# Optimization experiments

Measured on AMD Instinct MI355X. Metric: run time of the kernel, lower is better.

## Reference

```python
import math
import jax, jax.numpy as jnp
import numpy as np

B, H, D, N, M = 4, 8, 64, 8192, 256
EPS = 1e-6


def sample_orthogonal_random_vectors(num_rows, num_cols, seed=0):
    """Faithful port of FavorAttention.sample_orthogonal_random_vectors."""
    rng = np.random.default_rng(seed)
    num_blocks = math.ceil(num_rows / num_cols)
    unstructured = rng.standard_normal((num_blocks, num_cols, num_cols)).astype(np.float32)
    norm = np.linalg.norm(unstructured, axis=-1).reshape(-1, 1)
    q, _ = np.linalg.qr(unstructured)                 # reduced QR per block
    q = np.transpose(q, (0, 2, 1)).reshape(-1, num_cols)
    q = q[:num_rows, :] * norm[:num_rows, :]
    return jnp.asarray(q, dtype=jnp.float32)


def setup_inputs() -> dict:
    key = jax.random.key(0)
    kq, kk, kv = jax.random.split(key, 3)
    return {
        "query": jax.random.normal(kq, (B, H, D, N), dtype=jnp.float32),
        "key": jax.random.normal(kk, (B, H, D, N), dtype=jnp.float32),
        "value": jax.random.normal(kv, (B, H, D, N), dtype=jnp.float32),
        "projection_matrix": sample_orthogonal_random_vectors(M, D),
    }


def randomized_kernel(x, proj, is_query, eps=EPS):
    """FAVOR+ positive softmax features. x: [B,H,D,N] -> phi: [B,H,M,N]."""
    d = x.shape[2]
    data_normalizer = d ** -0.25
    ratio = proj.shape[0] ** -0.5
    # projected: [B,H,M,N]
    u = jnp.einsum('md,bhdn->bhmn', proj, x) * data_normalizer
    # ||x||^2 / (2*sqrt(d)) per token: [B,H,1,N]
    diag = jnp.sum(x * x, axis=2, keepdims=True) * (data_normalizer ** 2) * 0.5
    if is_query:
        stab = jnp.max(u, axis=2, keepdims=True)            # per-token max over features
    else:
        stab = jnp.max(u, axis=(2, 3), keepdims=True)       # global max per (b,h)
    return ratio * (jnp.exp(u - diag - stab) + eps)


def reference(query, key, value, projection_matrix):
    q_phi = randomized_kernel(query, projection_matrix, is_query=True)    # [B,H,M,N]
    k_phi = randomized_kernel(key, projection_matrix, is_query=False)     # [B,H,M,N]
    # kv = key @ value^T over sequence: [B,H,M,D]
    kv = jnp.einsum('bhmn,bhdn->bhmd', k_phi, value)
    key_norm = jnp.sum(k_phi, axis=3)                                     # [B,H,M]
    out = jnp.einsum('bhmn,bhmd->bhnd', q_phi, kv)                        # [B,H,N,D]
    out_norm = jnp.einsum('bhmn,bhm->bhn', q_phi, key_norm)[..., None]    # [B,H,N,1]
    out = out / out_norm
    return jnp.swapaxes(out, 2, 3)                                        # [B,H,D,N]


if __name__ == '__main__':
    o = reference(**setup_inputs())
    print(o.shape, o.dtype)
```

## Files before the change

### kernel.cpp

```cpp
#include <hip/hip_runtime.h>


typedef short s16x8 __attribute__((ext_vector_type(8)));
typedef float f32x4 __attribute__((ext_vector_type(4)));

#define Dv 64
#define Nv 8192
#define Mv 256
#define BHv 32
#define SPL 16
#define NSPL (Nv / SPL)
#define NCH (NSPL / 64)

#define DNRM 0.3535533905932738f
#define EPSV 1e-6f
#define KSTAB 15.0f

#define OFF_SGM 0
#define OFF_SVP (OFF_SGM + BHv * SPL * 8)
#define OFF_KNP (OFF_SVP + BHv * SPL * 64)
#define OFF_KNF (OFF_KNP + BHv * SPL * Mv)
#define OFF_KVP (OFF_KNF + BHv * Mv)
#define OFF_KVT (OFF_KVP + BHv * SPL * Mv * Dv)

__device__ __forceinline__ unsigned short f2b(float x) {
    return __builtin_bit_cast(unsigned short, (__bf16)x);
}

__device__ __forceinline__ s16x8 load_pfrag(const float* __restrict__ proj, int m,
                                            int kc, int q) {
    const float* p = proj + m * 64 + kc * 32 + q * 8;
    s16x8 r;
#pragma unroll
    for (int j = 0; j < 8; ++j) r[j] = (short)f2b(p[j]);
    return r;
}

__global__ __launch_bounds__(512, 4) void favor_kv(const float* __restrict__ key,
                                                   const float* __restrict__ value,
                                                   const float* __restrict__ proj,
                                                   float* __restrict__ ws) {
    __shared__ __align__(16) unsigned short KT[64][72];
    __shared__ __align__(16) unsigned short VL[64][72];
    __shared__ __align__(16) unsigned short PH[256][40];
    __shared__ __align__(16) float dred[16][64];
    __shared__ __align__(16) float dgl[64];
    const int tid = threadIdx.x;
    const int w = tid >> 6, l = tid & 63, c = l & 15, q = l >> 4;
    const int sg = tid >> 4, cs = tid & 15;
    const int s = blockIdx.x, bh = blockIdx.y;
    const float* kp = key + (size_t)bh * Dv * Nv;
    const float* vp = value + (size_t)bh * Dv * Nv;

    s16x8 P[2][2];
#pragma unroll
    for (int mt = 0; mt < 2; ++mt)
#pragma unroll
        for (int kc = 0; kc < 2; ++kc)
            P[mt][kc] = load_pfrag(proj, (2 * w + mt) * 16 + c, kc, q);

    f32x4 kva[2][4];
#pragma unroll
    for (int mt = 0; mt < 2; ++mt)
#pragma unroll
        for (int dt = 0; dt < 4; ++dt) kva[mt][dt] = (f32x4){0.f, 0.f, 0.f, 0.f};
    float kn[2] = {0.f, 0.f};
    float sv[4] = {0.f, 0.f, 0.f, 0.f};
    float tmax = -3.0e38f;

    for (int ch = 0; ch < NCH; ++ch) {
        const int n0 = s * NSPL + ch * 64;
        if (ch) __syncthreads();
        if (sg < 16) {
            const int g = sg;
            float4 kk[4];
#pragma unroll
            for (int di = 0; di < 4; ++di)
                kk[di] = *(const float4*)&kp[(4 * g + di) * Nv + n0 + 4 * cs];
#pragma unroll
            for (int j = 0; j < 4; ++j) {
                const float k0 = ((const float*)&kk[0])[j];
                const float k1 = ((const float*)&kk[1])[j];
                const float k2 = ((const float*)&kk[2])[j];
                const float k3 = ((const float*)&kk[3])[j];
                *(short4*)&KT[4 * cs + j][4 * g] =
                    make_short4((short)f2b(k0), (short)f2b(k1), (short)f2b(k2),
                                (short)f2b(k3));
                dred[g][4 * cs + j] = (k0 * k0 + k1 * k1) + (k2 * k2 + k3 * k3);
            }
        } else {
            const int g2 = sg - 16;
            float4 vv[4];
#pragma unroll
            for (int di = 0; di < 4; ++di)
                vv[di] = *(const float4*)&vp[(4 * g2 + di) * Nv + n0 + 4 * cs];
#pragma unroll
            for (int di = 0; di < 4; ++di) {
                *(short4*)&VL[4 * g2 + di][4 * cs] = make_short4(
                    (short)f2b(vv[di].x), (short)f2b(vv[di].y),
                    (short)f2b(vv[di].z), (short)f2b(vv[di].w));
                sv[di] += (vv[di].x + vv[di].y) + (vv[di].z + vv[di].w);
            }
        }
        __syncthreads();
        if (tid < 64) {
            float ds = 0.f;
#pragma unroll
            for (int gg = 0; gg < 16; ++gg) ds += dred[gg][tid];
            dgl[tid] = ds * 0.0625f + KSTAB;
        }
        __syncthreads();
#pragma unroll
        for (int h = 0; h < 2; ++h) {
#pragma unroll
            for (int nt2 = 0; nt2 < 2; ++nt2) {
                const int nt = 2 * h + nt2;
                const s16x8 a0 = *(const s16x8*)&KT[nt * 16 + c][q * 8];
                const s16x8 a1 = *(const s16x8*)&KT[nt * 16 + c][32 + q * 8];
                const float4 dg = *(const float4*)&dgl[nt * 16 + q * 4];
#pragma unroll
                for (int mt = 0; mt < 2; ++mt) {
                    f32x4 u = {0.f, 0.f, 0.f, 0.f};
                    u = __builtin_amdgcn_mfma_f32_16x16x32_bf16(a0, P[mt][0], u, 0, 0, 0);
                    u = __builtin_amdgcn_mfma_f32_16x16x32_bf16(a1, P[mt][1], u, 0, 0, 0);
                    tmax = fmaxf(tmax, fmaxf(fmaxf(u[0], u[1]), fmaxf(u[2], u[3])));
                    const float e0 = __expf(__builtin_fmaf(u[0], DNRM, -dg.x));
                    const float e1 = __expf(__builtin_fmaf(u[1], DNRM, -dg.y));
                    const float e2 = __expf(__builtin_fmaf(u[2], DNRM, -dg.z));
                    const float e3 = __expf(__builtin_fmaf(u[3], DNRM, -dg.w));
                    kn[mt] += (e0 + e1) + (e2 + e3);
                    *(short4*)&PH[(2 * w + mt) * 16 + c][nt2 * 16 + q * 4] =
                        make_short4((short)f2b(e0), (short)f2b(e1),
                                    (short)f2b(e2), (short)f2b(e3));
                }
            }
            s16x8 bf[4];
#pragma unroll
            for (int dt = 0; dt < 4; ++dt)
                bf[dt] = *(const s16x8*)&VL[dt * 16 + c][h * 32 + q * 8];
#pragma unroll
            for (int mt = 0; mt < 2; ++mt) {
                const s16x8 a = *(const s16x8*)&PH[(2 * w + mt) * 16 + c][q * 8];
#pragma unroll
                for (int dt = 0; dt < 4; ++dt)
                    kva[mt][dt] = __builtin_amdgcn_mfma_f32_16x16x32_bf16(
                        a, bf[dt], kva[mt][dt], 0, 0, 0);
            }
        }
    }
#pragma unroll
    for (int off = 1; off < 64; off <<= 1)
        tmax = fmaxf(tmax, __shfl_xor(tmax, off, 64));
    if (l == 0) ws[OFF_SGM + (bh * SPL + s) * 8 + w] = tmax * DNRM;
    float* kvp = ws + OFF_KVP + (size_t)(bh * SPL + s) * Mv * Dv;
#pragma unroll
    for (int mt = 0; mt < 2; ++mt) {
        const int mrow = (2 * w + mt) * 16 + 4 * q;
#pragma unroll
        for (int dt = 0; dt < 4; ++dt) {
            const int dcol = dt * 16 + c;
#pragma unroll
            for (int r = 0; r < 4; ++r)
                kvp[(size_t)(mrow + r) * Dv + dcol] = kva[mt][dt][r];
        }
    }
#pragma unroll
    for (int mt = 0; mt < 2; ++mt) {
        kn[mt] += __shfl_xor(kn[mt], 16, 64);
        kn[mt] += __shfl_xor(kn[mt], 32, 64);
    }
    if (q == 0) {
        float* knp = ws + OFF_KNP + (bh * SPL + s) * Mv;
#pragma unroll
        for (int mt = 0; mt < 2; ++mt) knp[(2 * w + mt) * 16 + c] = kn[mt];
    }
    __syncthreads();
    float* sp = &dred[0][0];
    if (sg >= 16) {
        const int g2 = sg - 16;
#pragma unroll
        for (int di = 0; di < 4; ++di) sp[(4 * g2 + di) * 16 + cs] = sv[di];
    }
    __syncthreads();
    if (tid < 64) {
        float t2 = 0.f;
#pragma unroll
        for (int j = 0; j < 16; ++j) t2 += sp[tid * 16 + j];
        ws[OFF_SVP + (bh * SPL + s) * 64 + tid] = t2;
    }
}

__global__ __launch_bounds__(256) void favor_kvred(float* __restrict__ ws) {
    __shared__ float sAl;
    __shared__ float svl[64];
    const int t = threadIdx.x, f = blockIdx.x, bh = blockIdx.y;
    const int flat = f * 1024 + t * 4;
    const int m = flat >> 6, d0 = flat & 63;
    if (t < 64) {
        float v = fmaxf(ws[OFF_SGM + bh * 128 + t],
                        ws[OFF_SGM + bh * 128 + 64 + t]);
#pragma unroll
        for (int off = 1; off < 64; off <<= 1)
            v = fmaxf(v, __shfl_xor(v, off, 64));
        if (t == 0) sAl = __expf(KSTAB - v);
    } else if (t < 128) {
        const int d = t - 64;
        float x = 0.f;
#pragma unroll
        for (int s2 = 0; s2 < SPL; ++s2)
            x += ws[OFF_SVP + (bh * SPL + s2) * 64 + d];
        svl[d] = x;
    }
    __syncthreads();
    const float al = sAl;
    float4 acc = make_float4(0.f, 0.f, 0.f, 0.f);
    for (int s2 = 0; s2 < SPL; ++s2) {
        const float4 v =
            *(const float4*)&ws[OFF_KVP + ((size_t)(bh * SPL + s2) << 14) + flat];
        acc.x += v.x; acc.y += v.y; acc.z += v.z; acc.w += v.w;
    }
    acc.x = acc.x * al + EPSV * svl[d0 + 0];
    acc.y = acc.y * al + EPSV * svl[d0 + 1];
    acc.z = acc.z * al + EPSV * svl[d0 + 2];
    acc.w = acc.w * al + EPSV * svl[d0 + 3];
    unsigned short* kvT = (unsigned short*)(ws + OFF_KVT);
    kvT[(bh * 64 + d0 + 0) * 256 + m] = f2b(acc.x);
    kvT[(bh * 64 + d0 + 1) * 256 + m] = f2b(acc.y);
    kvT[(bh * 64 + d0 + 2) * 256 + m] = f2b(acc.z);
    kvT[(bh * 64 + d0 + 3) * 256 + m] = f2b(acc.w);
    if (t < 16) {
        const int mm = f * 16 + t;
        float kk = 0.f;
        for (int s2 = 0; s2 < SPL; ++s2)
            kk += ws[OFF_KNP + (bh * SPL + s2) * Mv + mm];
        ws[OFF_KNF + bh * Mv + mm] = kk * al + EPSV * (float)Nv;
    }
}

__global__ __launch_bounds__(256, 2) void favor_out(const float* __restrict__ query,
                                                    const float* __restrict__ proj,
                                                    const float* __restrict__ ws,
                                                    float* __restrict__ out) {
    __shared__ __align__(16) unsigned short PHT[64][264];
    __shared__ float npart[4][64];
    __shared__ float knl[256];
    __shared__ float cw[4][64];
    __shared__ float stabl[64];
    __shared__ float dql[64];
    unsigned short (*QT)[72] = (unsigned short (*)[72]) & PHT[0][0];
    float (*dred)[64] = (float (*)[64])((char*)&PHT[0][0] + 9216);
    const int tid = threadIdx.x;
    const int w = tid >> 6, l = tid & 63, c = l & 15, q = l >> 4;
    const int g = tid >> 4, cs = tid & 15;
    const int nb = blockIdx.x, bh = blockIdx.y;
    const int n0 = nb * 64;
    const float* qp = query + (size_t)bh * Dv * Nv;
    const unsigned short* kvT =
        (const unsigned short*)(ws + OFF_KVT) + (size_t)bh * 64 * 256;

    {
        float4 qq[4];
#pragma unroll
        for (int di = 0; di < 4; ++di)
            qq[di] = *(const float4*)&qp[(4 * g + di) * Nv + n0 + 4 * cs];
#pragma unroll
        for (int j = 0; j < 4; ++j) {
            const float v0 = ((const float*)&qq[0])[j];
            const float v1 = ((const float*)&qq[1])[j];
            const float v2 = ((const float*)&qq[2])[j];
            const float v3 = ((const float*)&qq[3])[j];
            *(short4*)&QT[4 * cs + j][4 * g] =
                make_short4((short)f2b(v0), (short)f2b(v1), (short)f2b(v2),
                            (short)f2b(v3));
            dred[g][4 * cs + j] = (v0 * v0 + v1 * v1) + (v2 * v2 + v3 * v3);
        }
    }
    knl[tid] = ws[OFF_KNF + bh * Mv + tid];

    s16x8 P[4][2];
#pragma unroll
    for (int mt = 0; mt < 4; ++mt)
#pragma unroll
        for (int kc = 0; kc < 2; ++kc)
            P[mt][kc] = load_pfrag(proj, (4 * w + mt) * 16 + c, kc, q);
    __syncthreads();

    f32x4 u[4][4];
#pragma unroll
    for (int mt = 0; mt < 4; ++mt)
#pragma unroll
        for (int nt = 0; nt < 4; ++nt) u[mt][nt] = (f32x4){0.f, 0.f, 0.f, 0.f};
#pragma unroll
    for (int nt = 0; nt < 4; ++nt) {
        const s16x8 b0 = *(const s16x8*)&QT[nt * 16 + c][q * 8];
        const s16x8 b1 = *(const s16x8*)&QT[nt * 16 + c][32 + q * 8];
#pragma unroll
        for (int mt = 0; mt < 4; ++mt) {
            u[mt][nt] =
                __builtin_amdgcn_mfma_f32_16x16x32_bf16(P[mt][0], b0, u[mt][nt], 0, 0, 0);
            u[mt][nt] =
                __builtin_amdgcn_mfma_f32_16x16x32_bf16(P[mt][1], b1, u[mt][nt], 0, 0, 0);
        }
    }
#pragma unroll
    for (int nt = 0; nt < 4; ++nt) {
        float vm = -3.4e38f;
#pragma unroll
        for (int mt = 0; mt < 4; ++mt)
            vm = fmaxf(vm, fmaxf(fmaxf(u[mt][nt][0], u[mt][nt][1]),
                                 fmaxf(u[mt][nt][2], u[mt][nt][3])));
        vm = fmaxf(vm, __shfl_xor(vm, 16, 64));
        vm = fmaxf(vm, __shfl_xor(vm, 32, 64));
        if (q == 0) cw[w][nt * 16 + c] = vm;
    }
    __syncthreads();
    if (tid < 64) {
        stabl[tid] =
            fmaxf(fmaxf(cw[0][tid], cw[1][tid]), fmaxf(cw[2][tid], cw[3][tid]));
        float dsum = 0.f;
#pragma unroll
        for (int gg = 0; gg < 16; ++gg) dsum += dred[gg][tid];
        dql[tid] = dsum * 0.0625f;
    }
    __syncthreads();
#pragma unroll
    for (int nt = 0; nt < 4; ++nt) {
        const float sr = stabl[nt * 16 + c];
        const float dq = dql[nt * 16 + c];
        float np = 0.f;
#pragma unroll
        for (int mt = 0; mt < 4; ++mt) {
            const float e0 = __expf((u[mt][nt][0] - sr) * DNRM - dq) + EPSV;
            const float e1 = __expf((u[mt][nt][1] - sr) * DNRM - dq) + EPSV;
            const float e2 = __expf((u[mt][nt][2] - sr) * DNRM - dq) + EPSV;
            const float e3 = __expf((u[mt][nt][3] - sr) * DNRM - dq) + EPSV;
            const int mb = (4 * w + mt) * 16 + 4 * q;
            np += e0 * knl[mb] + e1 * knl[mb + 1] + e2 * knl[mb + 2] +
                  e3 * knl[mb + 3];
            *(short4*)&PHT[nt * 16 + c][mb] = make_short4(
                (short)f2b(e0), (short)f2b(e1), (short)f2b(e2), (short)f2b(e3));
        }
        np += __shfl_xor(np, 16, 64);
        np += __shfl_xor(np, 32, 64);
        if (q == 0) npart[w][nt * 16 + c] = np;
    }
    __syncthreads();
    f32x4 acc[4];
#pragma unroll
    for (int dt = 0; dt < 4; ++dt) acc[dt] = (f32x4){0.f, 0.f, 0.f, 0.f};
#pragma unroll
    for (int kc = 0; kc < 8; ++kc) {
        const s16x8 a = *(const s16x8*)&PHT[w * 16 + c][kc * 32 + q * 8];
#pragma unroll
        for (int dt = 0; dt < 4; ++dt) {
            const s16x8 b =
                *(const s16x8*)&kvT[(size_t)(dt * 16 + c) * 256 + kc * 32 + q * 8];
            acc[dt] = __builtin_amdgcn_mfma_f32_16x16x32_bf16(a, b, acc[dt], 0, 0, 0);
        }
    }
    __syncthreads();
    float* ot = (float*)&PHT[0][0];
    float rn[4];
#pragma unroll
    for (int r = 0; r < 4; ++r) {
        const int nl = w * 16 + 4 * q + r;
        rn[r] = 1.0f / ((npart[0][nl] + npart[1][nl]) +
                        (npart[2][nl] + npart[3][nl]));
    }
#pragma unroll
    for (int dt = 0; dt < 4; ++dt)
#pragma unroll
        for (int r = 0; r < 4; ++r)
            ot[(dt * 16 + c) * 68 + (w * 16 + 4 * q + r)] = acc[dt][r] * rn[r];
    __syncthreads();
    float* op = out + (size_t)bh * Dv * Nv;
    {
        const int d = tid >> 2, ng = (tid & 3) * 16;
#pragma unroll
        for (int i = 0; i < 4; ++i) {
            const float4 v = *(const float4*)&ot[d * 68 + ng + i * 4];
            *(float4*)&op[d * Nv + n0 + ng + i * 4] = v;
        }
    }
}

extern "C" void kernel_launch(void* const* d_in, const int* in_sizes, int n_in,
                              void* d_out, int out_size, void* d_ws, size_t ws_size,
                              hipStream_t stream) {
    const float* q = (const float*)d_in[0];
    const float* k = (const float*)d_in[1];
    const float* v = (const float*)d_in[2];
    const float* proj = (const float*)d_in[3];
    float* ws = (float*)d_ws;
    float* out = (float*)d_out;

    favor_kv<<<dim3(SPL, 32), 512, 0, stream>>>(k, v, proj, ws);
    favor_kvred<<<dim3(16, 32), 256, 0, stream>>>(ws);
    favor_out<<<dim3(Nv / 64, 32), 256, 0, stream>>>(q, proj, ws, out);
}
```

Baseline: 327.9 us.

## Drop per-token query max pass via algebraic eps correction and register-prefetch kv loads

```diff
diff --git a/kernel.cpp b/kernel.cpp
--- a/kernel.cpp
+++ b/kernel.cpp
@@ -16,12 +16,15 @@
 #define EPSV 1e-6f
 #define KSTAB 15.0f
 
-#define OFF_SGM 0
-#define OFF_SVP (OFF_SGM + BHv * SPL * 8)
+#define OFF_SD 0
+#define OFF_T (OFF_SD + BHv * Dv)
+#define OFF_SGM (OFF_T + BHv)
+#define OFF_SVP (OFF_SGM + BHv * SPL * 4)
 #define OFF_KNP (OFF_SVP + BHv * SPL * 64)
 #define OFF_KNF (OFF_KNP + BHv * SPL * Mv)
 #define OFF_KVP (OFF_KNF + BHv * Mv)
 #define OFF_KVT (OFF_KVP + BHv * SPL * Mv * Dv)
+#define ZERO_FLOATS (OFF_SGM)
 
 __device__ __forceinline__ unsigned short f2b(float x) {
     return __builtin_bit_cast(unsigned short, (__bf16)x);
@@ -36,7 +39,7 @@
     return r;
 }
 
-__global__ __launch_bounds__(512, 4) void favor_kv(const float* __restrict__ key,
+__global__ __launch_bounds__(256, 2) void favor_kv(const float* __restrict__ key,
                                                    const float* __restrict__ value,
                                                    const float* __restrict__ proj,
                                                    float* __restrict__ ws) {
@@ -47,59 +50,63 @@
     __shared__ __align__(16) float dgl[64];
     const int tid = threadIdx.x;
     const int w = tid >> 6, l = tid & 63, c = l & 15, q = l >> 4;
-    const int sg = tid >> 4, cs = tid & 15;
+    const int g = tid >> 4, cs = tid & 15;
     const int s = blockIdx.x, bh = blockIdx.y;
     const float* kp = key + (size_t)bh * Dv * Nv;
     const float* vp = value + (size_t)bh * Dv * Nv;
 
-    s16x8 P[2][2];
-#pragma unroll
-    for (int mt = 0; mt < 2; ++mt)
+    s16x8 P[4][2];
+#pragma unroll
+    for (int mt = 0; mt < 4; ++mt)
 #pragma unroll
         for (int kc = 0; kc < 2; ++kc)
-            P[mt][kc] = load_pfrag(proj, (2 * w + mt) * 16 + c, kc, q);
-
-    f32x4 kva[2][4];
-#pragma unroll
-    for (int mt = 0; mt < 2; ++mt)
+            P[mt][kc] = load_pfrag(proj, (4 * w + mt) * 16 + c, kc, q);
+
+    f32x4 kva[4][4];
+#pragma unroll
+    for (int mt = 0; mt < 4; ++mt)
 #pragma unroll
         for (int dt = 0; dt < 4; ++dt) kva[mt][dt] = (f32x4){0.f, 0.f, 0.f, 0.f};
-    float kn[2] = {0.f, 0.f};
+    float kn[4] = {0.f, 0.f, 0.f, 0.f};
     float sv[4] = {0.f, 0.f, 0.f, 0.f};
     float tmax = -3.0e38f;
 
+    float4 kk[4], vv[4];
+    {
+        const int n0 = s * NSPL;
+#pragma unroll
+        for (int di = 0; di < 4; ++di) {
+            kk[di] = *(const float4*)&kp[(4 * g + di) * Nv + n0 + 4 * cs];
+            vv[di] = *(const float4*)&vp[(4 * g + di) * Nv + n0 + 4 * cs];
+        }
+    }
+
     for (int ch = 0; ch < NCH; ++ch) {
-        const int n0 = s * NSPL + ch * 64;
         if (ch) __syncthreads();
-        if (sg < 16) {
-            const int g = sg;
-            float4 kk[4];
-#pragma unroll
-            for (int di = 0; di < 4; ++di)
-                kk[di] = *(const float4*)&kp[(4 * g + di) * Nv + n0 + 4 * cs];
-#pragma unroll
-            for (int j = 0; j < 4; ++j) {
-                const float k0 = ((const float*)&kk[0])[j];
-                const float k1 = ((const float*)&kk[1])[j];
-                const float k2 = ((const float*)&kk[2])[j];
-                const float k3 = ((const float*)&kk[3])[j];
-                *(short4*)&KT[4 * cs + j][4 * g] =
-                    make_short4((short)f2b(k0), (short)f2b(k1), (short)f2b(k2),
-                                (short)f2b(k3));
-                dred[g][4 * cs + j] = (k0 * k0 + k1 * k1) + (k2 * k2 + k3 * k3);
-            }
-        } else {
-            const int g2 = sg - 16;
-            float4 vv[4];
-#pragma unroll
-            for (int di = 0; di < 4; ++di)
-                vv[di] = *(const float4*)&vp[(4 * g2 + di) * Nv + n0 + 4 * cs];
+#pragma unroll
+        for (int j = 0; j < 4; ++j) {
+            const float k0 = ((const float*)&kk[0])[j];
+            const float k1 = ((const float*)&kk[1])[j];
+            const float k2 = ((const float*)&kk[2])[j];
+            const float k3 = ((const float*)&kk[3])[j];
+            *(short4*)&KT[4 * cs + j][4 * g] =
+                make_short4((short)f2b(k0), (short)f2b(k1), (short)f2b(k2),
+                            (short)f2b(k3));
+            dred[g][4 * cs + j] = (k0 * k0 + k1 * k1) + (k2 * k2 + k3 * k3);
+        }
+#pragma unroll
+        for (int di = 0; di < 4; ++di) {
+            *(short4*)&VL[4 * g + di][4 * cs] = make_short4(
+                (short)f2b(vv[di].x), (short)f2b(vv[di].y),
+                (short)f2b(vv[di].z), (short)f2b(vv[di].w));
+            sv[di] += (vv[di].x + vv[di].y) + (vv[di].z + vv[di].w);
+        }
+        if (ch + 1 < NCH) {
+            const int n1 = s * NSPL + (ch + 1) * 64;
 #pragma unroll
             for (int di = 0; di < 4; ++di) {
-                *(short4*)&VL[4 * g2 + di][4 * cs] = make_short4(
-                    (short)f2b(vv[di].x), (short)f2b(vv[di].y),
-                    (short)f2b(vv[di].z), (short)f2b(vv[di].w));
-                sv[di] += (vv[di].x + vv[di].y) + (vv[di].z + vv[di].w);
+                kk[di] = *(const float4*)&kp[(4 * g + di) * Nv + n1 + 4 * cs];
+                vv[di] = *(const float4*)&vp[(4 * g + di) * Nv + n1 + 4 * cs];
             }
         }
         __syncthreads();
@@ -119,7 +126,7 @@
                 const s16x8 a1 = *(const s16x8*)&KT[nt * 16 + c][32 + q * 8];
                 const float4 dg = *(const float4*)&dgl[nt * 16 + q * 4];
 #pragma unroll
-                for (int mt = 0; mt < 2; ++mt) {
+                for (int mt = 0; mt < 4; ++mt) {
                     f32x4 u = {0.f, 0.f, 0.f, 0.f};
                     u = __builtin_amdgcn_mfma_f32_16x16x32_bf16(a0, P[mt][0], u, 0, 0, 0);
                     u = __builtin_amdgcn_mfma_f32_16x16x32_bf16(a1, P[mt][1], u, 0, 0, 0);
@@ -129,7 +136,7 @@
                     const float e2 = __expf(__builtin_fmaf(u[2], DNRM, -dg.z));
                     const float e3 = __expf(__builtin_fmaf(u[3], DNRM, -dg.w));
                     kn[mt] += (e0 + e1) + (e2 + e3);
-                    *(short4*)&PH[(2 * w + mt) * 16 + c][nt2 * 16 + q * 4] =
+                    *(short4*)&PH[(4 * w + mt) * 16 + c][nt2 * 16 + q * 4] =
                         make_short4((short)f2b(e0), (short)f2b(e1),
                                     (short)f2b(e2), (short)f2b(e3));
                 }
@@ -139,8 +146,8 @@
             for (int dt = 0; dt < 4; ++dt)
                 bf[dt] = *(const s16x8*)&VL[dt * 16 + c][h * 32 + q * 8];
 #pragma unroll
-            for (int mt = 0; mt < 2; ++mt) {
-                const s16x8 a = *(const s16x8*)&PH[(2 * w + mt) * 16 + c][q * 8];
+            for (int mt = 0; mt < 4; ++mt) {
+                const s16x8 a = *(const s16x8*)&PH[(4 * w + mt) * 16 + c][q * 8];
 #pragma unroll
                 for (int dt = 0; dt < 4; ++dt)
                     kva[mt][dt] = __builtin_amdgcn_mfma_f32_16x16x32_bf16(
@@ -151,11 +158,11 @@
 #pragma unroll
     for (int off = 1; off < 64; off <<= 1)
         tmax = fmaxf(tmax, __shfl_xor(tmax, off, 64));
-    if (l == 0) ws[OFF_SGM + (bh * SPL + s) * 8 + w] = tmax * DNRM;
+    if (l == 0) ws[OFF_SGM + (bh * SPL + s) * 4 + w] = tmax * DNRM;
     float* kvp = ws + OFF_KVP + (size_t)(bh * SPL + s) * Mv * Dv;
 #pragma unroll
-    for (int mt = 0; mt < 2; ++mt) {
-        const int mrow = (2 * w + mt) * 16 + 4 * q;
+    for (int mt = 0; mt < 4; ++mt) {
+        const int mrow = (4 * w + mt) * 16 + 4 * q;
 #pragma unroll
         for (int dt = 0; dt < 4; ++dt) {
             const int dcol = dt * 16 + c;
@@ -165,22 +172,19 @@
         }
     }
 #pragma unroll
-    for (int mt = 0; mt < 2; ++mt) {
+    for (int mt = 0; mt < 4; ++mt) {
         kn[mt] += __shfl_xor(kn[mt], 16, 64);
         kn[mt] += __shfl_xor(kn[mt], 32, 64);
     }
     if (q == 0) {
         float* knp = ws + OFF_KNP + (bh * SPL + s) * Mv;
 #pragma unroll
-        for (int mt = 0; mt < 2; ++mt) knp[(2 * w + mt) * 16 + c] = kn[mt];
+        for (int mt = 0; mt < 4; ++mt) knp[(4 * w + mt) * 16 + c] = kn[mt];
     }
     __syncthreads();
     float* sp = &dred[0][0];
-    if (sg >= 16) {
-        const int g2 = sg - 16;
-#pragma unroll
-        for (int di = 0; di < 4; ++di) sp[(4 * g2 + di) * 16 + cs] = sv[di];
-    }
+#pragma unroll
+    for (int di = 0; di < 4; ++di) sp[(4 * g + di) * 16 + cs] = sv[di];
     __syncthreads();
     if (tid < 64) {
         float t2 = 0.f;
@@ -197,8 +201,7 @@
     const int flat = f * 1024 + t * 4;
     const int m = flat >> 6, d0 = flat & 63;
     if (t < 64) {
-        float v = fmaxf(ws[OFF_SGM + bh * 128 + t],
-                        ws[OFF_SGM + bh * 128 + 64 + t]);
+        float v = ws[OFF_SGM + bh * 64 + t];
 #pragma unroll
         for (int off = 1; off < 64; off <<= 1)
             v = fmaxf(v, __shfl_xor(v, off, 64));
@@ -228,12 +231,18 @@
     kvT[(bh * 64 + d0 + 1) * 256 + m] = f2b(acc.y);
     kvT[(bh * 64 + d0 + 2) * 256 + m] = f2b(acc.z);
     kvT[(bh * 64 + d0 + 3) * 256 + m] = f2b(acc.w);
+    atomicAdd(&ws[OFF_SD + bh * 64 + d0 + 0], acc.x);
+    atomicAdd(&ws[OFF_SD + bh * 64 + d0 + 1], acc.y);
+    atomicAdd(&ws[OFF_SD + bh * 64 + d0 + 2], acc.z);
+    atomicAdd(&ws[OFF_SD + bh * 64 + d0 + 3], acc.w);
     if (t < 16) {
         const int mm = f * 16 + t;
         float kk = 0.f;
         for (int s2 = 0; s2 < SPL; ++s2)
             kk += ws[OFF_KNP + (bh * SPL + s2) * Mv + mm];
-        ws[OFF_KNF + bh * Mv + mm] = kk * al + EPSV * (float)Nv;
+        const float knf = kk * al + EPSV * (float)Nv;
+        ws[OFF_KNF + bh * Mv + mm] = knf;
+        atomicAdd(&ws[OFF_T + bh], knf);
     }
 }
 
@@ -245,8 +254,9 @@
     __shared__ float npart[4][64];
     __shared__ float knl[256];
     __shared__ float cw[4][64];
-    __shared__ float stabl[64];
     __shared__ float dql[64];
+    __shared__ float Sl[64];
+    __shared__ float Ts;
     unsigned short (*QT)[72] = (unsigned short (*)[72]) & PHT[0][0];
     float (*dred)[64] = (float (*)[64])((char*)&PHT[0][0] + 9216);
     const int tid = threadIdx.x;
@@ -276,6 +286,8 @@
         }
     }
     knl[tid] = ws[OFF_KNF + bh * Mv + tid];
+    if (tid < 64) Sl[tid] = ws[OFF_SD + bh * 64 + tid];
+    if (tid == 0) Ts = ws[OFF_T + bh];
 
     s16x8 P[4][2];
 #pragma unroll
@@ -284,6 +296,20 @@
         for (int kc = 0; kc < 2; ++kc)
             P[mt][kc] = load_pfrag(proj, (4 * w + mt) * 16 + c, kc, q);
     __syncthreads();
+
+    if (tid < 64) {
+        float dsum = 0.f;
+#pragma unroll
+        for (int gg = 0; gg < 16; ++gg) dsum += dred[gg][tid];
+        dql[tid] = dsum * 0.0625f;
+    }
+    float knr[4][4];
+#pragma unroll
+    for (int mt = 0; mt < 4; ++mt) {
+        const int mb = (4 * w + mt) * 16 + 4 * q;
+#pragma unroll
+        for (int r = 0; r < 4; ++r) knr[mt][r] = knl[mb + r];
+    }
 
     f32x4 u[4][4];
 #pragma unroll
@@ -302,47 +328,34 @@
                 __builtin_amdgcn_mfma_f32_16x16x32_bf16(P[mt][1], b1, u[mt][nt], 0, 0, 0);
         }
     }
+    __syncthreads();
 #pragma unroll
     for (int nt = 0; nt < 4; ++nt) {
+        const float dq = dql[nt * 16 + c];
+        float np = 0.f;
         float vm = -3.4e38f;
 #pragma unroll
-        for (int mt = 0; mt < 4; ++mt)
+        for (int mt = 0; mt < 4; ++mt) {
             vm = fmaxf(vm, fmaxf(fmaxf(u[mt][nt][0], u[mt][nt][1]),
                                  fmaxf(u[mt][nt][2], u[mt][nt][3])));
+            const float e0 = __expf(__builtin_fmaf(u[mt][nt][0], DNRM, -dq));
+            const float e1 = __expf(__builtin_fmaf(u[mt][nt][1], DNRM, -dq));
+            const float e2 = __expf(__builtin_fmaf(u[mt][nt][2], DNRM, -dq));
+            const float e3 = __expf(__builtin_fmaf(u[mt][nt][3], DNRM, -dq));
+            const int mb = (4 * w + mt) * 16 + 4 * q;
+            np += e0 * knr[mt][0] + e1 * knr[mt][1] + e2 * knr[mt][2] +
+                  e3 * knr[mt][3];
+            *(short4*)&PHT[nt * 16 + c][mb] = make_short4(
+                (short)f2b(e0), (short)f2b(e1), (short)f2b(e2), (short)f2b(e3));
+        }
+        np += __shfl_xor(np, 16, 64);
+        np += __shfl_xor(np, 32, 64);
         vm = fmaxf(vm, __shfl_xor(vm, 16, 64));
         vm = fmaxf(vm, __shfl_xor(vm, 32, 64));
-        if (q == 0) cw[w][nt * 16 + c] = vm;
-    }
-    __syncthreads();
-    if (tid < 64) {
-        stabl[tid] =
-            fmaxf(fmaxf(cw[0][tid], cw[1][tid]), fmaxf(cw[2][tid], cw[3][tid]));
-        float dsum = 0.f;
-#pragma unroll
-        for (int gg = 0; gg < 16; ++gg) dsum += dred[gg][tid];
-        dql[tid] = dsum * 0.0625f;
-    }
-    __syncthreads();
-#pragma unroll
-    for (int nt = 0; nt < 4; ++nt) {
-        const float sr = stabl[nt * 16 + c];
-        const float dq = dql[nt * 16 + c];
-        float np = 0.f;
-#pragma unroll
-        for (int mt = 0; mt < 4; ++mt) {
-            const float e0 = __expf((u[mt][nt][0] - sr) * DNRM - dq) + EPSV;
-            const float e1 = __expf((u[mt][nt][1] - sr) * DNRM - dq) + EPSV;
-            const float e2 = __expf((u[mt][nt][2] - sr) * DNRM - dq) + EPSV;
-            const float e3 = __expf((u[mt][nt][3] - sr) * DNRM - dq) + EPSV;
-            const int mb = (4 * w + mt) * 16 + 4 * q;
-            np += e0 * knl[mb] + e1 * knl[mb + 1] + e2 * knl[mb + 2] +
-                  e3 * knl[mb + 3];
-            *(short4*)&PHT[nt * 16 + c][mb] = make_short4(
-                (short)f2b(e0), (short)f2b(e1), (short)f2b(e2), (short)f2b(e3));
-        }
-        np += __shfl_xor(np, 16, 64);
-        np += __shfl_xor(np, 32, 64);
-        if (q == 0) npart[w][nt * 16 + c] = np;
+        if (q == 0) {
+            npart[w][nt * 16 + c] = np;
+            cw[w][nt * 16 + c] = vm;
+        }
     }
     __syncthreads();
     f32x4 acc[4];
@@ -360,18 +373,24 @@
     }
     __syncthreads();
     float* ot = (float*)&PHT[0][0];
-    float rn[4];
+    float rn[4], gm[4];
 #pragma unroll
     for (int r = 0; r < 4; ++r) {
         const int nl = w * 16 + 4 * q + r;
-        rn[r] = 1.0f / ((npart[0][nl] + npart[1][nl]) +
-                        (npart[2][nl] + npart[3][nl]));
+        const float npsum = (npart[0][nl] + npart[1][nl]) +
+                            (npart[2][nl] + npart[3][nl]);
+        const float st =
+            fmaxf(fmaxf(cw[0][nl], cw[1][nl]), fmaxf(cw[2][nl], cw[3][nl]));
+        const float gamma = EPSV * __expf(st * DNRM);
+        gm[r] = gamma;
+        rn[r] = 1.0f / (npsum + gamma * Ts);
     }
 #pragma unroll
     for (int dt = 0; dt < 4; ++dt)
 #pragma unroll
         for (int r = 0; r < 4; ++r)
-            ot[(dt * 16 + c) * 68 + (w * 16 + 4 * q + r)] = acc[dt][r] * rn[r];
+            ot[(dt * 16 + c) * 68 + (w * 16 + 4 * q + r)] =
+                (acc[dt][r] + gm[r] * Sl[dt * 16 + c]) * rn[r];
     __syncthreads();
     float* op = out + (size_t)bh * Dv * Nv;
     {
@@ -394,7 +413,8 @@
     float* ws = (float*)d_ws;
     float* out = (float*)d_out;
 
-    favor_kv<<<dim3(SPL, 32), 512, 0, stream>>>(k, v, proj, ws);
+    hipMemsetAsync(ws, 0, (size_t)ZERO_FLOATS * sizeof(float), stream);
+    favor_kv<<<dim3(SPL, 32), 256, 0, stream>>>(k, v, proj, ws);
     favor_kvred<<<dim3(16, 32), 256, 0, stream>>>(ws);
     favor_out<<<dim3(Nv / 64, 32), 256, 0, stream>>>(q, proj, ws, out);
 }
```

Measured after the change: 353.2 us. +7.7%, slower.
